# Optimization experiments

Measured on AMD Instinct MI355X. Metric: run time of the kernel, lower is better.

The kernel has to match this reference:

```python
import jax, jax.numpy as jnp
import numpy as np


def setup_inputs() -> dict:
    key = jax.random.key(0)
    kq, kk, kv = jax.random.split(key, 3)
    B, H, S, D = 4, 16, 2048, 64
    q = jax.random.normal(kq, (B, H, S, D), dtype=jnp.float32)
    k = jax.random.normal(kk, (B, H, S, D), dtype=jnp.float32)
    v = jax.random.normal(kv, (B, H, S, D), dtype=jnp.float32)
    return {"q": q, "k": k, "v": v}


def reference(q, k, v):
    # Flash-attention math (causal=True, softmax_scale = 1/sqrt(head_dim)).
    D = q.shape[-1]
    scale = 1.0 / np.sqrt(D).astype(np.float32)
    # scores: [B, H, Sq, Sk]
    scores = jnp.einsum('bhqd,bhkd->bhqk', q, k) * scale
    Sq, Sk = scores.shape[-2], scores.shape[-1]
    causal_mask = jnp.tril(jnp.ones((Sq, Sk), dtype=bool))  # [Sq, Sk]
    neg_inf = jnp.asarray(jnp.finfo(scores.dtype).min, scores.dtype)
    scores = jnp.where(causal_mask, scores, neg_inf)
    probs = jax.nn.softmax(scores, axis=-1)
    out = jnp.einsum('bhqk,bhkd->bhqd', probs, v)
    return out
```

## Files before the change

kernel.cpp:

```cpp
#include <hip/hip_runtime.h>
#include <hip/hip_bf16.h>

#define S_LEN 2048
#define DH 64
#define QBLK 128
#define KVBLK 64
#define LDPK 72
#define LDPV 68

typedef __attribute__((ext_vector_type(4))) float f32x4;
typedef __attribute__((ext_vector_type(8))) short short8v;
typedef __attribute__((ext_vector_type(4))) unsigned uint4v;
typedef __attribute__((ext_vector_type(2))) unsigned uint2v;

__device__ __forceinline__ unsigned cvt_pk(float a, float b) {
    unsigned r;
    asm("v_cvt_pk_bf16_f32 %0, %1, %2" : "=v"(r) : "v"(a), "v"(b));
    return r;
}

__global__ __launch_bounds__(512) void fa_fwd_kernel(
    const float* __restrict__ Q, const float* __restrict__ K,
    const float* __restrict__ V, float* __restrict__ O)
{
    const int tid  = threadIdx.x;
    const int lane = tid & 63;
    const int w    = tid >> 6;
    const int bh   = blockIdx.x & 63;
    const int p    = blockIdx.x >> 6;

    const size_t base = (size_t)bh * S_LEN * DH;
    const float* Qg = Q + base;
    const float* Kg = K + base;
    const float* Vg = V + base;
    float*       Og = O + base;

    __shared__ __align__(16) short K_lds[2][KVBLK][LDPK];
    __shared__ __align__(16) short V_lds[2][DH][LDPV];

    const int lr = lane & 15;
    const int lg = lane >> 4;
    const int kr = tid >> 3;
    const int dc = (tid & 7) * 8;
    const int vd = tid & 63;
    const int vg = tid >> 6;

    unsigned kpfu[4], vpf[4];

    auto prefetch = [&](int kvb) {
        const float* kp = Kg + (size_t)(kvb + kr) * DH + dc;
        f32x4 a = *(const f32x4*)kp;
        f32x4 b = *(const f32x4*)(kp + 4);
        kpfu[0] = cvt_pk(a[0], a[1]);
        kpfu[1] = cvt_pk(a[2], a[3]);
        kpfu[2] = cvt_pk(b[0], b[1]);
        kpfu[3] = cvt_pk(b[2], b[3]);
        #pragma unroll
        for (int i = 0; i < 4; ++i) {
            int kv = vg * 8 + i * 2;
            float x = Vg[(size_t)(kvb + kv) * DH + vd];
            float y = Vg[(size_t)(kvb + kv + 1) * DH + vd];
            vpf[i] = cvt_pk(x, y);
        }
    };

    auto stage = [&](int b) {
        uint4v u = {kpfu[0], kpfu[1], kpfu[2], kpfu[3]};
        *(uint4v*)&K_lds[b][kr][dc] = u;
        #pragma unroll
        for (int i = 0; i < 4; ++i) {
            int kv = vg * 8 + i * 2;
            *(unsigned*)((char*)&V_lds[b][0][0] + vd * (LDPV * 2) + kv * 2) = vpf[i];
        }
    };

    const float qscale = 0.125f * 1.44269504088896340736f;

    prefetch(0);
    stage(0);
    int cur = 0;
    __syncthreads();

    #pragma unroll 1
    for (int t = 0; t < 2; ++t) {
        const int qb = (t == 0) ? (15 - p) : p;
        const int q0 = qb * QBLK + w * 16;
        const int kv_end = (qb + 1) * QBLK;

        short8v qfrag[2];
        #pragma unroll
        for (int kf = 0; kf < 2; ++kf) {
            const float* qp = Qg + (size_t)(q0 + lr) * DH + kf * 32 + lg * 8;
            f32x4 a = *(const f32x4*)qp;
            f32x4 b = *(const f32x4*)(qp + 4);
            uint4v u;
            u[0] = cvt_pk(a[0] * qscale, a[1] * qscale);
            u[1] = cvt_pk(a[2] * qscale, a[3] * qscale);
            u[2] = cvt_pk(b[0] * qscale, b[1] * qscale);
            u[3] = cvt_pk(b[2] * qscale, b[3] * qscale);
            qfrag[kf] = __builtin_bit_cast(short8v, u);
        }

        f32x4 o_acc[4];
        #pragma unroll
        for (int i = 0; i < 4; ++i)
            o_acc[i] = (f32x4){0.f, 0.f, 0.f, 0.f};
        float m_run = -1e30f, l_run = 0.f;

        #pragma unroll 1
        for (int kvb = 0; kvb < kv_end; kvb += KVBLK) {
            int nkv = kvb + KVBLK;
            bool have = true;
            if (nkv >= kv_end) { if (t == 0) nkv = 0; else have = false; }
            if (have) prefetch(nkv);

            if (kvb <= q0) {
                const short (*Kc)[LDPK] = K_lds[cur];
                const char* Vc = (const char*)&V_lds[cur][0][0];

                f32x4 s_acc[4];
                #pragma unroll
                for (int kt = 0; kt < 4; ++kt)
                    s_acc[kt] = (f32x4){0.f, 0.f, 0.f, 0.f};

                __builtin_amdgcn_s_setprio(1);
                #pragma unroll
                for (int kt = 0; kt < 4; ++kt) {
                    short8v kf0 = *(const short8v*)&Kc[kt * 16 + lr][lg * 8];
                    short8v kf1 = *(const short8v*)&Kc[kt * 16 + lr][32 + lg * 8];
                    s_acc[kt] = __builtin_amdgcn_mfma_f32_16x16x32_bf16(
                        kf0, qfrag[0], s_acc[kt], 0, 0, 0);
                    s_acc[kt] = __builtin_amdgcn_mfma_f32_16x16x32_bf16(
                        kf1, qfrag[1], s_acc[kt], 0, 0, 0);
                }
                __builtin_amdgcn_s_setprio(0);

                const int qrow = q0 + lr;
                if (kvb + KVBLK - 1 > q0) {
                    #pragma unroll
                    for (int kt = 0; kt < 4; ++kt)
                        #pragma unroll
                        for (int r = 0; r < 4; ++r) {
                            int kvv = kvb + kt * 16 + lg * 4 + r;
                            if (kvv > qrow) s_acc[kt][r] = -1e30f;
                        }
                }

                float tmax = -1e30f;
                #pragma unroll
                for (int kt = 0; kt < 4; ++kt)
                    #pragma unroll
                    for (int r = 0; r < 4; ++r)
                        tmax = fmaxf(tmax, s_acc[kt][r]);
                tmax = fmaxf(tmax, __shfl_xor(tmax, 16));
                tmax = fmaxf(tmax, __shfl_xor(tmax, 32));

                if (!__all(tmax <= m_run + 8.0f)) {
                    float mnew = fmaxf(m_run, tmax);
                    float corr = __builtin_amdgcn_exp2f(m_run - mnew);
                    m_run = mnew;
                    l_run *= corr;
                    #pragma unroll
                    for (int r = 0; r < 4; ++r) {
                        float c = __shfl(corr, 4 * lg + r);
                        #pragma unroll
                        for (int dt = 0; dt < 4; ++dt)
                            o_acc[dt][r] *= c;
                    }
                }

                float rsum = 0.f;
                #pragma unroll
                for (int kt = 0; kt < 4; ++kt)
                    #pragma unroll
                    for (int r = 0; r < 4; ++r) {
                        float pe = __builtin_amdgcn_exp2f(s_acc[kt][r] - m_run);
                        s_acc[kt][r] = pe;
                        rsum += pe;
                    }
                rsum += __shfl_xor(rsum, 16);
                rsum += __shfl_xor(rsum, 32);
                l_run += rsum;

                short8v pa[2];
                #pragma unroll
                for (int kf = 0; kf < 2; ++kf) {
                    uint4v u;
                    u[0] = cvt_pk(s_acc[2 * kf][0],     s_acc[2 * kf][1]);
                    u[1] = cvt_pk(s_acc[2 * kf][2],     s_acc[2 * kf][3]);
                    u[2] = cvt_pk(s_acc[2 * kf + 1][0], s_acc[2 * kf + 1][1]);
                    u[3] = cvt_pk(s_acc[2 * kf + 1][2], s_acc[2 * kf + 1][3]);
                    pa[kf] = __builtin_bit_cast(short8v, u);
                }

                __builtin_amdgcn_s_setprio(1);
                #pragma unroll
                for (int dt = 0; dt < 4; ++dt) {
                    const char* vrow = Vc + (dt * 16 + lr) * (LDPV * 2);
                    #pragma unroll
                    for (int kf = 0; kf < 2; ++kf) {
                        uint2v lo = *(const uint2v*)(vrow + (kf * 32 + 4 * lg) * 2);
                        uint2v hi = *(const uint2v*)(vrow + (kf * 32 + 16 + 4 * lg) * 2);
                        uint4v u = {lo[0], lo[1], hi[0], hi[1]};
                        short8v vv = __builtin_bit_cast(short8v, u);
                        o_acc[dt] = __builtin_amdgcn_mfma_f32_16x16x32_bf16(
                            pa[kf], vv, o_acc[dt], 0, 0, 0);
                    }
                }
                __builtin_amdgcn_s_setprio(0);
            }

            if (have) {
                stage(cur ^ 1);
                __syncthreads();
            }
            cur ^= 1;
        }

        #pragma unroll
        for (int r = 0; r < 4; ++r) {
            float ls = __shfl(l_run, 4 * lg + r);
            float inv = 1.0f / ls;
            int qrow = q0 + lg * 4 + r;
            float* op = Og + (size_t)qrow * DH + lr;
            #pragma unroll
            for (int dt = 0; dt < 4; ++dt)
                op[dt * 16] = o_acc[dt][r] * inv;
        }
    }
}

extern "C" void kernel_launch(void* const* d_in, const int* in_sizes, int n_in,
                              void* d_out, int out_size, void* d_ws, size_t ws_size,
                              hipStream_t stream) {
    const float* q = (const float*)d_in[0];
    const float* k = (const float*)d_in[1];
    const float* v = (const float*)d_in[2];
    float* out = (float*)d_out;
    fa_fwd_kernel<<<dim3(512), dim3(512), 0, stream>>>(q, k, v, out);
}
```

Before: 79.02 us.

## Switch attention to 32x32x16 MFMA with 32-row waves and 256-thread blocks

```diff
diff --git a/kernel.cpp b/kernel.cpp
--- a/kernel.cpp
+++ b/kernel.cpp
@@ -8,10 +8,11 @@
 #define LDPK 72
 #define LDPV 68
 
-typedef __attribute__((ext_vector_type(4))) float f32x4;
-typedef __attribute__((ext_vector_type(8))) short short8v;
-typedef __attribute__((ext_vector_type(4))) unsigned uint4v;
-typedef __attribute__((ext_vector_type(2))) unsigned uint2v;
+typedef __attribute__((ext_vector_type(4)))  float f32x4;
+typedef __attribute__((ext_vector_type(16))) float f32x16;
+typedef __attribute__((ext_vector_type(8)))  short short8v;
+typedef __attribute__((ext_vector_type(4)))  unsigned uint4v;
+typedef __attribute__((ext_vector_type(2)))  unsigned uint2v;
 
 __device__ __forceinline__ unsigned cvt_pk(float a, float b) {
     unsigned r;
@@ -19,7 +20,7 @@
     return r;
 }
 
-__global__ __launch_bounds__(512) void fa_fwd_kernel(
+__global__ __launch_bounds__(256) void fa_fwd_kernel(
     const float* __restrict__ Q, const float* __restrict__ K,
     const float* __restrict__ V, float* __restrict__ O)
 {
@@ -38,26 +39,28 @@
     __shared__ __align__(16) short K_lds[2][KVBLK][LDPK];
     __shared__ __align__(16) short V_lds[2][DH][LDPV];
 
-    const int lr = lane & 15;
-    const int lg = lane >> 4;
-    const int kr = tid >> 3;
-    const int dc = (tid & 7) * 8;
+    const int q  = lane & 31;
+    const int hi = lane >> 5;
+    const int kr = tid >> 2;
+    const int dc = (tid & 3) * 16;
     const int vd = tid & 63;
     const int vg = tid >> 6;
 
-    unsigned kpfu[4], vpf[4];
+    unsigned kpfu[8], vpf[8];
 
     auto prefetch = [&](int kvb) {
         const float* kp = Kg + (size_t)(kvb + kr) * DH + dc;
         f32x4 a = *(const f32x4*)kp;
         f32x4 b = *(const f32x4*)(kp + 4);
-        kpfu[0] = cvt_pk(a[0], a[1]);
-        kpfu[1] = cvt_pk(a[2], a[3]);
-        kpfu[2] = cvt_pk(b[0], b[1]);
-        kpfu[3] = cvt_pk(b[2], b[3]);
-        #pragma unroll
-        for (int i = 0; i < 4; ++i) {
-            int kv = vg * 8 + i * 2;
+        f32x4 c = *(const f32x4*)(kp + 8);
+        f32x4 d = *(const f32x4*)(kp + 12);
+        kpfu[0] = cvt_pk(a[0], a[1]); kpfu[1] = cvt_pk(a[2], a[3]);
+        kpfu[2] = cvt_pk(b[0], b[1]); kpfu[3] = cvt_pk(b[2], b[3]);
+        kpfu[4] = cvt_pk(c[0], c[1]); kpfu[5] = cvt_pk(c[2], c[3]);
+        kpfu[6] = cvt_pk(d[0], d[1]); kpfu[7] = cvt_pk(d[2], d[3]);
+        #pragma unroll
+        for (int i = 0; i < 8; ++i) {
+            int kv = vg * 16 + i * 2;
             float x = Vg[(size_t)(kvb + kv) * DH + vd];
             float y = Vg[(size_t)(kvb + kv + 1) * DH + vd];
             vpf[i] = cvt_pk(x, y);
@@ -65,11 +68,13 @@
     };
 
     auto stage = [&](int b) {
-        uint4v u = {kpfu[0], kpfu[1], kpfu[2], kpfu[3]};
-        *(uint4v*)&K_lds[b][kr][dc] = u;
-        #pragma unroll
-        for (int i = 0; i < 4; ++i) {
-            int kv = vg * 8 + i * 2;
+        uint4v u0 = {kpfu[0], kpfu[1], kpfu[2], kpfu[3]};
+        uint4v u1 = {kpfu[4], kpfu[5], kpfu[6], kpfu[7]};
+        *(uint4v*)&K_lds[b][kr][dc]     = u0;
+        *(uint4v*)&K_lds[b][kr][dc + 8] = u1;
+        #pragma unroll
+        for (int i = 0; i < 8; ++i) {
+            int kv = vg * 16 + i * 2;
             *(unsigned*)((char*)&V_lds[b][0][0] + vd * (LDPV * 2) + kv * 2) = vpf[i];
         }
     };
@@ -84,13 +89,13 @@
     #pragma unroll 1
     for (int t = 0; t < 2; ++t) {
         const int qb = (t == 0) ? (15 - p) : p;
-        const int q0 = qb * QBLK + w * 16;
+        const int q0 = qb * QBLK + w * 32;
         const int kv_end = (qb + 1) * QBLK;
 
-        short8v qfrag[2];
-        #pragma unroll
-        for (int kf = 0; kf < 2; ++kf) {
-            const float* qp = Qg + (size_t)(q0 + lr) * DH + kf * 32 + lg * 8;
+        short8v qfrag[4];
+        #pragma unroll
+        for (int ds = 0; ds < 4; ++ds) {
+            const float* qp = Qg + (size_t)(q0 + q) * DH + ds * 16 + hi * 8;
             f32x4 a = *(const f32x4*)qp;
             f32x4 b = *(const f32x4*)(qp + 4);
             uint4v u;
@@ -98,13 +103,12 @@
             u[1] = cvt_pk(a[2] * qscale, a[3] * qscale);
             u[2] = cvt_pk(b[0] * qscale, b[1] * qscale);
             u[3] = cvt_pk(b[2] * qscale, b[3] * qscale);
-            qfrag[kf] = __builtin_bit_cast(short8v, u);
-        }
-
-        f32x4 o_acc[4];
-        #pragma unroll
-        for (int i = 0; i < 4; ++i)
-            o_acc[i] = (f32x4){0.f, 0.f, 0.f, 0.f};
+            qfrag[ds] = __builtin_bit_cast(short8v, u);
+        }
+
+        f32x16 o_acc[2];
+        o_acc[0] = (f32x16)(0.f);
+        o_acc[1] = (f32x16)(0.f);
         float m_run = -1e30f, l_run = 0.f;
 
         #pragma unroll 1
@@ -118,42 +122,40 @@
                 const short (*Kc)[LDPK] = K_lds[cur];
                 const char* Vc = (const char*)&V_lds[cur][0][0];
 
-                f32x4 s_acc[4];
-                #pragma unroll
-                for (int kt = 0; kt < 4; ++kt)
-                    s_acc[kt] = (f32x4){0.f, 0.f, 0.f, 0.f};
+                f32x16 s_acc[2];
+                s_acc[0] = (f32x16)(0.f);
+                s_acc[1] = (f32x16)(0.f);
 
                 __builtin_amdgcn_s_setprio(1);
                 #pragma unroll
-                for (int kt = 0; kt < 4; ++kt) {
-                    short8v kf0 = *(const short8v*)&Kc[kt * 16 + lr][lg * 8];
-                    short8v kf1 = *(const short8v*)&Kc[kt * 16 + lr][32 + lg * 8];
-                    s_acc[kt] = __builtin_amdgcn_mfma_f32_16x16x32_bf16(
-                        kf0, qfrag[0], s_acc[kt], 0, 0, 0);
-                    s_acc[kt] = __builtin_amdgcn_mfma_f32_16x16x32_bf16(
-                        kf1, qfrag[1], s_acc[kt], 0, 0, 0);
+                for (int ds = 0; ds < 4; ++ds) {
+                    #pragma unroll
+                    for (int kt = 0; kt < 2; ++kt) {
+                        short8v kf = *(const short8v*)&Kc[kt * 32 + q][ds * 16 + hi * 8];
+                        s_acc[kt] = __builtin_amdgcn_mfma_f32_32x32x16_bf16(
+                            kf, qfrag[ds], s_acc[kt], 0, 0, 0);
+                    }
                 }
                 __builtin_amdgcn_s_setprio(0);
 
-                const int qrow = q0 + lr;
+                const int qrow = q0 + q;
                 if (kvb + KVBLK - 1 > q0) {
                     #pragma unroll
-                    for (int kt = 0; kt < 4; ++kt)
+                    for (int kt = 0; kt < 2; ++kt)
                         #pragma unroll
-                        for (int r = 0; r < 4; ++r) {
-                            int kvv = kvb + kt * 16 + lg * 4 + r;
-                            if (kvv > qrow) s_acc[kt][r] = -1e30f;
+                        for (int r = 0; r < 16; ++r) {
+                            int kv = kvb + kt * 32 + (r & 3) + 8 * (r >> 2) + 4 * hi;
+                            if (kv > qrow) s_acc[kt][r] = -1e30f;
                         }
                 }
 
-                float tmax = -1e30f;
-                #pragma unroll
-                for (int kt = 0; kt < 4; ++kt)
-                    #pragma unroll
-                    for (int r = 0; r < 4; ++r)
-                        tmax = fmaxf(tmax, s_acc[kt][r]);
-                tmax = fmaxf(tmax, __shfl_xor(tmax, 16));
-                tmax = fmaxf(tmax, __shfl_xor(tmax, 32));
+                float tl = -1e30f;
+                #pragma unroll
+                for (int kt = 0; kt < 2; ++kt)
+                    #pragma unroll
+                    for (int r = 0; r < 16; ++r)
+                        tl = fmaxf(tl, s_acc[kt][r]);
+                float tmax = fmaxf(tl, __shfl_xor(tl, 32));
 
                 if (!__all(tmax <= m_run + 8.0f)) {
                     float mnew = fmaxf(m_run, tmax);
@@ -161,50 +163,47 @@
                     m_run = mnew;
                     l_run *= corr;
                     #pragma unroll
-                    for (int r = 0; r < 4; ++r) {
-                        float c = __shfl(corr, 4 * lg + r);
+                    for (int dt = 0; dt < 2; ++dt)
                         #pragma unroll
-                        for (int dt = 0; dt < 4; ++dt)
-                            o_acc[dt][r] *= c;
-                    }
+                        for (int r = 0; r < 16; ++r)
+                            o_acc[dt][r] *= corr;
                 }
 
                 float rsum = 0.f;
                 #pragma unroll
-                for (int kt = 0; kt < 4; ++kt)
-                    #pragma unroll
-                    for (int r = 0; r < 4; ++r) {
+                for (int kt = 0; kt < 2; ++kt)
+                    #pragma unroll
+                    for (int r = 0; r < 16; ++r) {
                         float pe = __builtin_amdgcn_exp2f(s_acc[kt][r] - m_run);
                         s_acc[kt][r] = pe;
                         rsum += pe;
                     }
-                rsum += __shfl_xor(rsum, 16);
                 rsum += __shfl_xor(rsum, 32);
                 l_run += rsum;
 
-                short8v pa[2];
-                #pragma unroll
-                for (int kf = 0; kf < 2; ++kf) {
-                    uint4v u;
-                    u[0] = cvt_pk(s_acc[2 * kf][0],     s_acc[2 * kf][1]);
-                    u[1] = cvt_pk(s_acc[2 * kf][2],     s_acc[2 * kf][3]);
-                    u[2] = cvt_pk(s_acc[2 * kf + 1][0], s_acc[2 * kf + 1][1]);
-                    u[3] = cvt_pk(s_acc[2 * kf + 1][2], s_acc[2 * kf + 1][3]);
-                    pa[kf] = __builtin_bit_cast(short8v, u);
-                }
+                unsigned pk_[2][8];
+                #pragma unroll
+                for (int kt = 0; kt < 2; ++kt)
+                    #pragma unroll
+                    for (int m = 0; m < 8; ++m)
+                        pk_[kt][m] = cvt_pk(s_acc[kt][2 * m], s_acc[kt][2 * m + 1]);
 
                 __builtin_amdgcn_s_setprio(1);
                 #pragma unroll
-                for (int dt = 0; dt < 4; ++dt) {
-                    const char* vrow = Vc + (dt * 16 + lr) * (LDPV * 2);
-                    #pragma unroll
-                    for (int kf = 0; kf < 2; ++kf) {
-                        uint2v lo = *(const uint2v*)(vrow + (kf * 32 + 4 * lg) * 2);
-                        uint2v hi = *(const uint2v*)(vrow + (kf * 32 + 16 + 4 * lg) * 2);
-                        uint4v u = {lo[0], lo[1], hi[0], hi[1]};
-                        short8v vv = __builtin_bit_cast(short8v, u);
-                        o_acc[dt] = __builtin_amdgcn_mfma_f32_16x16x32_bf16(
-                            pa[kf], vv, o_acc[dt], 0, 0, 0);
+                for (int s = 0; s < 4; ++s) {
+                    const int kt = s >> 1, bofs = 4 * (s & 1);
+                    uint4v bu = {pk_[kt][bofs], pk_[kt][bofs + 1],
+                                 pk_[kt][bofs + 2], pk_[kt][bofs + 3]};
+                    short8v pb = __builtin_bit_cast(short8v, bu);
+                    #pragma unroll
+                    for (int dt = 0; dt < 2; ++dt) {
+                        const char* vrow = Vc + (size_t)(dt * 32 + q) * (LDPV * 2);
+                        uint2v lo = *(const uint2v*)(vrow + (16 * s + 4 * hi) * 2);
+                        uint2v h2 = *(const uint2v*)(vrow + (16 * s + 8 + 4 * hi) * 2);
+                        uint4v au = {lo[0], lo[1], h2[0], h2[1]};
+                        short8v va = __builtin_bit_cast(short8v, au);
+                        o_acc[dt] = __builtin_amdgcn_mfma_f32_32x32x16_bf16(
+                            va, pb, o_acc[dt], 0, 0, 0);
                     }
                 }
                 __builtin_amdgcn_s_setprio(0);
@@ -217,15 +216,16 @@
             cur ^= 1;
         }
 
-        #pragma unroll
-        for (int r = 0; r < 4; ++r) {
-            float ls = __shfl(l_run, 4 * lg + r);
-            float inv = 1.0f / ls;
-            int qrow = q0 + lg * 4 + r;
-            float* op = Og + (size_t)qrow * DH + lr;
+        float inv = 1.0f / l_run;
+        float* orow = Og + (size_t)(q0 + q) * DH;
+        #pragma unroll
+        for (int dt = 0; dt < 2; ++dt) {
             #pragma unroll
-            for (int dt = 0; dt < 4; ++dt)
-                op[dt * 16] = o_acc[dt][r] * inv;
+            for (int g = 0; g < 4; ++g) {
+                f32x4 ov = {o_acc[dt][4 * g] * inv,     o_acc[dt][4 * g + 1] * inv,
+                            o_acc[dt][4 * g + 2] * inv, o_acc[dt][4 * g + 3] * inv};
+                *(f32x4*)(orow + dt * 32 + 8 * g + 4 * hi) = ov;
+            }
         }
     }
 }
@@ -237,5 +237,5 @@
     const float* k = (const float*)d_in[1];
     const float* v = (const float*)d_in[2];
     float* out = (float*)d_out;
-    fa_fwd_kernel<<<dim3(512), dim3(512), 0, stream>>>(q, k, v, out);
+    fa_fwd_kernel<<<dim3(512), dim3(256), 0, stream>>>(q, k, v, out);
 }
```

New measurement: 86.96 us. +10.1%, slower.
